# Performance work log

Hardware: AMD Instinct MI355X
Metric: run time of the kernel (lower is better)

The kernel has to match this reference:

```python
import jax, jax.numpy as jnp
import numpy as np

PAD_POS = 100.0   # column 0: sigmoid(100) ~ 1  (identity factor on left)
PAD_NEG = -100.0  # column 1: 1 - sigmoid(-100) ~ 1 (identity factor on right)


def setup_inputs() -> dict:
    key = jax.random.key(0)
    k1, k2 = jax.random.split(key)
    B, V = 2048, 32768
    scores = jax.random.normal(k1, (B, V), dtype=jnp.float32)
    class_indices = jax.random.randint(k2, (B,), 0, V, dtype=jnp.int64)
    return {"scores": scores, "class_indices": class_indices}


def _tree_indices(class_indices, code_len):
    """Vectorized version of the host-side per-bit tree traversal.
    Returns left_t, right_t of shape [B, code_len] (int32 gather indices)."""
    ci = class_indices.astype(jnp.int32)
    shifts = jnp.arange(code_len - 1, -1, -1, dtype=jnp.int32)
    bits = (ci[:, None] >> shifts[None, :]) & 1  # [B, L], MSB first

    def step(idx, bit):  # idx: [B] current tree node index into padded_scores
        right_branch = bit == 1
        left = jnp.where(right_branch, 0, idx)    # 0 -> sigmoid(100) ~ 1
        right = jnp.where(right_branch, idx, 1)   # 1 -> 1 - sigmoid(-100) ~ 1
        nidx = jnp.where(right_branch, 2 * idx, 2 * idx - 1)
        return nidx, (left, right)

    init = jnp.full(ci.shape, 2, dtype=jnp.int32)
    _, (left_t, right_t) = jax.lax.scan(step, init, bits.T)  # [L, B]
    return left_t.T, right_t.T


def reference(scores, class_indices):
    B, V = scores.shape
    code_len = int(np.ceil(np.log2(V)))
    padded = jnp.concatenate(
        [jnp.full((B, 1), PAD_POS, scores.dtype),
         jnp.full((B, 1), PAD_NEG, scores.dtype),
         scores], axis=1)  # [B, V+2]
    left_t, right_t = _tree_indices(class_indices, code_len)  # [B, L]
    left_part = jax.nn.sigmoid(jnp.take_along_axis(padded, left_t, axis=1))
    right_part = 1.0 - jax.nn.sigmoid(jnp.take_along_axis(padded, right_t, axis=1))
    probs = jnp.prod(left_part, axis=1) * jnp.prod(right_part, axis=1)  # [B]
    return jnp.sum(-jnp.log(probs)) / B
```

## Files before the change

kernel.cpp:

```cpp
#include <hip/hip_runtime.h>


#define B_ROWS   2048
#define V_COLS   32768
#define CODE_LEN 15
#define NBLOCKS  64
#define NTHREADS 512
#define MAGIC    0x5CA1AB1Eu

__device__ __forceinline__ float softplus_f(float x) {
    return fmaxf(x, 0.0f) + log1pf(expf(-fabsf(x)));
}

__global__ void __launch_bounds__(NTHREADS)
hsm_onenode_kernel(const float* __restrict__ scores,
                   const int* __restrict__ class_indices,
                   float* __restrict__ out,
                   unsigned long long* __restrict__ slots) {
    const int g = blockIdx.x * NTHREADS + threadIdx.x;
    const int b = g >> 4;
    const int t = g & 15;

    float acc = 0.0f;
    if (t < CODE_LEN) {
        const int ci = class_indices[b];
        const float s = scores[(size_t)b * V_COLS +
                               ((1 << t) - 1) + (ci >> (CODE_LEN - t))];
        const int bit = (ci >> (CODE_LEN - 1 - t)) & 1;
        acc = softplus_f(bit ? s : -s);
    }

#pragma unroll
    for (int off = 32; off > 0; off >>= 1)
        acc += __shfl_down(acc, off);

    __shared__ float lds[NTHREADS / 64];
    if ((threadIdx.x & 63) == 0)
        lds[threadIdx.x >> 6] = acc;
    __syncthreads();

    if (threadIdx.x == 0) {
        float p = 0.0f;
#pragma unroll
        for (int w = 0; w < NTHREADS / 64; ++w)
            p += lds[w];
        const unsigned long long enc =
            ((unsigned long long)MAGIC << 32) | (unsigned long long)__float_as_uint(p);
        __hip_atomic_store(&slots[blockIdx.x], enc,
                           __ATOMIC_RELEASE, __HIP_MEMORY_SCOPE_AGENT);
    }

    if (blockIdx.x == 0 && threadIdx.x < 64) {
        unsigned long long e;
        bool ok;
        do {
            e = __hip_atomic_load(&slots[threadIdx.x],
                                  __ATOMIC_ACQUIRE, __HIP_MEMORY_SCOPE_AGENT);
            ok = ((unsigned int)(e >> 32) == MAGIC);
        } while (!__all(ok));

        float v = __uint_as_float((unsigned int)e);
#pragma unroll
        for (int off = 32; off > 0; off >>= 1)
            v += __shfl_down(v, off);
        if (threadIdx.x == 0)
            out[0] = v * (1.0f / (float)B_ROWS);
    }
}

extern "C" void kernel_launch(void* const* d_in, const int* in_sizes, int n_in,
                              void* d_out, int out_size, void* d_ws, size_t ws_size,
                              hipStream_t stream) {
    const float* scores        = (const float*)d_in[0];
    const int*   class_indices = (const int*)d_in[1];
    float*       out           = (float*)d_out;
    unsigned long long* slots  = (unsigned long long*)d_ws;

    hsm_onenode_kernel<<<NBLOCKS, NTHREADS, 0, stream>>>(scores, class_indices,
                                                         out, slots);
}
```

Measured before the change: 9.420 us.

## Publish per-wave partials and use a dedicated finisher block for reduction

Each wave writes its own partial sum to a flagged slot, removing the LDS reduction and block barrier. An extra block is launched solely to poll all 512 slots and produce the final mean, instead of work block 0 doing the spin-wait. This trades a barrier for more polling loads and an additional block.

```diff
diff --git a/kernel.cpp b/kernel.cpp
--- a/kernel.cpp
+++ b/kernel.cpp
@@ -4,8 +4,9 @@
 #define B_ROWS   2048
 #define V_COLS   32768
 #define CODE_LEN 15
-#define NBLOCKS  64
+#define NWORK    64
 #define NTHREADS 512
+#define NSLOTS   (NWORK * 8)
 #define MAGIC    0x5CA1AB1Eu
 
 __device__ __forceinline__ float softplus_f(float x) {
@@ -17,52 +18,55 @@
                    const int* __restrict__ class_indices,
                    float* __restrict__ out,
                    unsigned long long* __restrict__ slots) {
-    const int g = blockIdx.x * NTHREADS + threadIdx.x;
-    const int b = g >> 4;
-    const int t = g & 15;
+    if (blockIdx.x < NWORK) {
+        const int g = blockIdx.x * NTHREADS + threadIdx.x;
+        const int b = g >> 4;
+        const int t = g & 15;
 
-    float acc = 0.0f;
-    if (t < CODE_LEN) {
-        const int ci = class_indices[b];
-        const float s = scores[(size_t)b * V_COLS +
-                               ((1 << t) - 1) + (ci >> (CODE_LEN - t))];
-        const int bit = (ci >> (CODE_LEN - 1 - t)) & 1;
-        acc = softplus_f(bit ? s : -s);
-    }
+        float acc = 0.0f;
+        if (t < CODE_LEN) {
+            const int ci = class_indices[b];
+            const float s = scores[(size_t)b * V_COLS +
+                                   ((1 << t) - 1) + (ci >> (CODE_LEN - t))];
+            const int bit = (ci >> (CODE_LEN - 1 - t)) & 1;
+            acc = softplus_f(bit ? s : -s);
+        }
 
 #pragma unroll
-    for (int off = 32; off > 0; off >>= 1)
-        acc += __shfl_down(acc, off);
+        for (int off = 32; off > 0; off >>= 1)
+            acc += __shfl_down(acc, off);
 
-    __shared__ float lds[NTHREADS / 64];
-    if ((threadIdx.x & 63) == 0)
-        lds[threadIdx.x >> 6] = acc;
-    __syncthreads();
-
-    if (threadIdx.x == 0) {
-        float p = 0.0f;
-#pragma unroll
-        for (int w = 0; w < NTHREADS / 64; ++w)
-            p += lds[w];
-        const unsigned long long enc =
-            ((unsigned long long)MAGIC << 32) | (unsigned long long)__float_as_uint(p);
-        __hip_atomic_store(&slots[blockIdx.x], enc,
-                           __ATOMIC_RELEASE, __HIP_MEMORY_SCOPE_AGENT);
-    }
-
-    if (blockIdx.x == 0 && threadIdx.x < 64) {
-        unsigned long long e;
+        if ((threadIdx.x & 63) == 0) {
+            const int slot = blockIdx.x * 8 + (threadIdx.x >> 6);
+            const unsigned long long enc =
+                ((unsigned long long)MAGIC << 32) |
+                (unsigned long long)__float_as_uint(acc);
+            __hip_atomic_store(&slots[slot], enc,
+                               __ATOMIC_RELEASE, __HIP_MEMORY_SCOPE_AGENT);
+        }
+    } else if (threadIdx.x < 64) {
+        unsigned long long e[8];
         bool ok;
         do {
-            e = __hip_atomic_load(&slots[threadIdx.x],
-                                  __ATOMIC_ACQUIRE, __HIP_MEMORY_SCOPE_AGENT);
-            ok = ((unsigned int)(e >> 32) == MAGIC);
+            ok = true;
+#pragma unroll
+            for (int w = 0; w < 8; ++w) {
+                e[w] = __hip_atomic_load(&slots[threadIdx.x + 64 * w],
+                                         __ATOMIC_ACQUIRE,
+                                         __HIP_MEMORY_SCOPE_AGENT);
+                ok = ok && ((unsigned int)(e[w] >> 32) == MAGIC);
+            }
         } while (!__all(ok));
 
-        float v = __uint_as_float((unsigned int)e);
+        float v = 0.0f;
+#pragma unroll
+        for (int w = 0; w < 8; ++w)
+            v += __uint_as_float((unsigned int)e[w]);
+
 #pragma unroll
         for (int off = 32; off > 0; off >>= 1)
             v += __shfl_down(v, off);
+
         if (threadIdx.x == 0)
             out[0] = v * (1.0f / (float)B_ROWS);
     }
@@ -76,6 +80,6 @@
     float*       out           = (float*)d_out;
     unsigned long long* slots  = (unsigned long long*)d_ws;
 
-    hsm_onenode_kernel<<<NBLOCKS, NTHREADS, 0, stream>>>(scores, class_indices,
-                                                         out, slots);
+    hsm_onenode_kernel<<<NWORK + 1, NTHREADS, 0, stream>>>(scores, class_indices,
+                                                           out, slots);
 }
```

Measured after the change: 10.79 us. 1.15x slower.
